# Optimization experiments

Measured on AMD Instinct MI355X. Metric: run time of the kernel, lower is better.

Reference implementation:

```python
import jax, jax.numpy as jnp
import numpy as np

DEPTH = 9            # tree depth -> 2**DEPTH-1 = 511 nodes, 255 internal
ENSEMBLE = 16
CLASS_NUM = 10
IN_DIM = 784
HID = 128            # encode_feature_dimension for arch='mlp'
BATCH = 8192
INTERNAL = 2 ** (DEPTH - 1) - 1   # 255
TOTAL = 2 ** DEPTH - 1            # 511


def setup_inputs() -> dict:
    key = jax.random.key(0)
    ks = jax.random.split(key, 7)
    X = jax.random.normal(ks[0], (BATCH, IN_DIM), dtype=jnp.float32)
    W1 = jax.random.normal(ks[1], (IN_DIM, HID), dtype=jnp.float32) * 0.02
    b1 = jnp.zeros((HID,), jnp.float32)
    W2 = jax.random.normal(ks[2], (HID, CLASS_NUM), dtype=jnp.float32) * 0.02
    b2 = jnp.zeros((CLASS_NUM,), jnp.float32)
    # xavier-uniform style node weights: Linear(HID, 1) per internal node per tree
    limit = float(np.sqrt(6.0 / (HID + 1)))
    nodeW = jax.random.uniform(ks[3], (ENSEMBLE, INTERNAL, HID), jnp.float32, -limit, limit)
    nodeb = jnp.zeros((ENSEMBLE, INTERNAL), jnp.float32)
    return {"X": X, "W1": W1, "b1": b1, "W2": W2, "b2": b2, "nodeW": nodeW, "nodeb": nodeb}


def _tree_paths(feats, nodeW, nodeb):
    # feats: [B, HID]; nodeW: [T, I, HID]; nodeb: [T, I]
    # decisions for ALL internal nodes in one batched GEMM
    dec = jax.nn.sigmoid(jnp.einsum('bd,tid->tib', feats, nodeW) + nodeb[:, :, None])  # [T, I, B]
    T, I, B = dec.shape
    results = jnp.ones((T, TOTAL, B), feats.dtype)
    # level-wise parallel prefix product down the tree (loop over DEPTH-1 levels only)
    for lvl in range(DEPTH - 1):
        start = 2 ** lvl - 1
        cnt = 2 ** lvl
        parent = results[:, start:start + cnt]          # [T, cnt, B]
        d = dec[:, start:start + cnt]                   # [T, cnt, B]
        # children of parent i are 2i+1 (left: *d) and 2i+2 (right: *(1-d)),
        # contiguous + interleaved starting at 2*start+1 = 2**(lvl+1)-1
        children = jnp.stack([parent * d, parent * (1.0 - d)], axis=2).reshape(T, 2 * cnt, B)
        results = results.at[:, 2 * start + 1: 2 * start + 1 + 2 * cnt].set(children)
    return results  # [T, TOTAL, B]


def reference(X, W1, b1, W2, b2, nodeW, nodeb):
    feats = jax.nn.relu(X @ W1 + b1)          # encoder embedding [B, HID]
    prediction = feats @ W2 + b2              # auxiliary predictor [B, CLASS_NUM]
    all_results = _tree_paths(feats, nodeW, nodeb)  # [T, 2**D-1, B]
    return prediction, all_results
```

## Files before the change

kernel.cpp:

```cpp
#include <hip/hip_runtime.h>
#include <hip/hip_bf16.h>

#define BATCH 8192
#define IN_DIM 784
#define HID 128
#define CLS 10
#define ENSEMBLE 16
#define INTERNAL 255
#define TOTAL 511
#define KPAD 800

typedef __attribute__((ext_vector_type(8))) short short8;
typedef __attribute__((ext_vector_type(4))) float floatx4;


__global__ void convert_kernel(const float* __restrict__ X,
                               const float* __restrict__ W1,
                               const float* __restrict__ nodeW,
                               __hip_bfloat16* __restrict__ Xbf,
                               __hip_bfloat16* __restrict__ W1T,
                               __hip_bfloat16* __restrict__ nWbf) {
  const int N1 = BATCH * KPAD;
  const int N2 = HID * KPAD;
  const int N3 = ENSEMBLE * 256 * HID;
  const int total = N1 + N2 + N3;
  for (int i = blockIdx.x * blockDim.x + threadIdx.x; i < total;
       i += gridDim.x * blockDim.x) {
    if (i < N1) {
      int b = i / KPAD, k = i - b * KPAD;
      float v = (k < IN_DIM) ? X[b * IN_DIM + k] : 0.0f;
      Xbf[i] = __float2bfloat16(v);
    } else if (i < N1 + N2) {
      int j = i - N1;
      int c = j / KPAD, k = j - c * KPAD;
      float v = (k < IN_DIM) ? W1[k * HID + c] : 0.0f;
      W1T[j] = __float2bfloat16(v);
    } else {
      int j = i - N1 - N2;
      int t = j / (256 * HID);
      int r = j - t * 256 * HID;
      int ii = r / HID;
      int d = r - ii * HID;
      float v = (ii < INTERNAL) ? nodeW[(t * INTERNAL + ii) * HID + d] : 0.0f;
      nWbf[j] = __float2bfloat16(v);
    }
  }
}

__global__ __launch_bounds__(128) void feats_kernel(
    const __hip_bfloat16* __restrict__ Xbf,
    const __hip_bfloat16* __restrict__ W1T,
    const float* __restrict__ b1,
    float* __restrict__ feats,
    __hip_bfloat16* __restrict__ featsbf) {
  const int wave = threadIdx.x >> 6;
  const int lane = threadIdx.x & 63;
  const int lo = lane & 15;
  const int q = lane >> 4;
  const int m0 = blockIdx.x * 32 + wave * 16;

  floatx4 acc[8];
#pragma unroll
  for (int nt = 0; nt < 8; nt++) acc[nt] = (floatx4){0.f, 0.f, 0.f, 0.f};

  const short* Xp = (const short*)Xbf;
  const short* Wp = (const short*)W1T;
  for (int ks = 0; ks < KPAD / 32; ks++) {
    const int koff = ks * 32 + q * 8;
    short8 a = *(const short8*)(Xp + (size_t)(m0 + lo) * KPAD + koff);
#pragma unroll
    for (int nt = 0; nt < 8; nt++) {
      short8 b = *(const short8*)(Wp + (size_t)(nt * 16 + lo) * KPAD + koff);
      acc[nt] = __builtin_amdgcn_mfma_f32_16x16x32_bf16(a, b, acc[nt], 0, 0, 0);
    }
  }
#pragma unroll
  for (int nt = 0; nt < 8; nt++) {
    const int c = nt * 16 + lo;
    const float bias = b1[c];
#pragma unroll
    for (int r = 0; r < 4; r++) {
      const int brow = m0 + q * 4 + r;
      float v = acc[nt][r] + bias;
      v = fmaxf(v, 0.0f);
      feats[(size_t)brow * HID + c] = v;
      featsbf[(size_t)brow * HID + c] = __float2bfloat16(v);
    }
  }
}

__global__ void pred_kernel(const float* __restrict__ feats,
                            const float* __restrict__ W2,
                            const float* __restrict__ b2,
                            float* __restrict__ out) {
  int gid = blockIdx.x * blockDim.x + threadIdx.x;
  if (gid >= BATCH * CLS) return;
  int b = gid / CLS, c = gid - b * CLS;
  float acc = b2[c];
  const float* fr = feats + (size_t)b * HID;
#pragma unroll 4
  for (int k = 0; k < HID; k++) acc += fr[k] * W2[k * CLS + c];
  out[gid] = acc;
}

__global__ __launch_bounds__(256) void tree_kernel(
    const __hip_bfloat16* __restrict__ featsbf,
    const __hip_bfloat16* __restrict__ nWbf,
    const float* __restrict__ nodeb,
    float* __restrict__ out ) {
  __shared__ float dec_s[INTERNAL * 32];
  __shared__ float P_s[INTERNAL * 32];

  const int t = blockIdx.y;
  const int b0 = blockIdx.x * 32;
  const int tid = threadIdx.x;
  const int wave = tid >> 6;
  const int lane = tid & 63;
  const int lo = lane & 15;
  const int q = lane >> 4;

  const short* Fp = (const short*)featsbf;
  const short* Np = (const short*)nWbf;

  short8 bfr[2][4];
#pragma unroll
  for (int nt = 0; nt < 2; nt++)
#pragma unroll
    for (int ks = 0; ks < 4; ks++)
      bfr[nt][ks] =
          *(const short8*)(Fp + (size_t)(b0 + nt * 16 + lo) * HID + ks * 32 + q * 8);

#pragma unroll
  for (int mt = 0; mt < 4; mt++) {
    const int ibase = wave * 64 + mt * 16;
    floatx4 acc0 = {0.f, 0.f, 0.f, 0.f};
    floatx4 acc1 = {0.f, 0.f, 0.f, 0.f};
#pragma unroll
    for (int ks = 0; ks < 4; ks++) {
      short8 a = *(const short8*)(Np + (size_t)(t * 256 + ibase + lo) * HID +
                                  ks * 32 + q * 8);
      acc0 = __builtin_amdgcn_mfma_f32_16x16x32_bf16(a, bfr[0][ks], acc0, 0, 0, 0);
      acc1 = __builtin_amdgcn_mfma_f32_16x16x32_bf16(a, bfr[1][ks], acc1, 0, 0, 0);
    }
#pragma unroll
    for (int r = 0; r < 4; r++) {
      const int iloc = ibase + q * 4 + r;
      if (iloc < INTERNAL) {
        const float nb = nodeb[t * INTERNAL + iloc];
        const float x0 = acc0[r] + nb;
        const float x1 = acc1[r] + nb;
        dec_s[iloc * 32 + lo] = 1.0f / (1.0f + __expf(-x0));
        dec_s[iloc * 32 + 16 + lo] = 1.0f / (1.0f + __expf(-x1));
      }
    }
  }
  __syncthreads();

  float* outT = out + (size_t)t * TOTAL * BATCH + b0;
  if (tid < 32) {
    P_s[tid] = 1.0f;
    outT[tid] = 1.0f;
  }
  __syncthreads();

  for (int lvl = 0; lvl < 8; lvl++) {
    const int start = (1 << lvl) - 1;
    const int nchild = 2 << lvl;
    const int items = nchild * 32;
    for (int it = tid; it < items; it += 256) {
      const int c = it >> 5;
      const int b = it & 31;
      const int pnode = start + (c >> 1);
      const float d = dec_s[pnode * 32 + b];
      const float pv = P_s[pnode * 32 + b];
      const float val = pv * ((c & 1) ? (1.0f - d) : d);
      const int cnode = 2 * start + 1 + c;
      outT[(size_t)cnode * BATCH + b] = val;
      if (cnode < INTERNAL) P_s[cnode * 32 + b] = val;
    }
    __syncthreads();
  }
}

extern "C" void kernel_launch(void* const* d_in, const int* in_sizes, int n_in,
                              void* d_out, int out_size, void* d_ws, size_t ws_size,
                              hipStream_t stream) {
  const float* X = (const float*)d_in[0];
  const float* W1 = (const float*)d_in[1];
  const float* b1 = (const float*)d_in[2];
  const float* W2 = (const float*)d_in[3];
  const float* b2 = (const float*)d_in[4];
  const float* nodeW = (const float*)d_in[5];
  const float* nodeb = (const float*)d_in[6];

  float* pred_out = (float*)d_out;
  float* results_out = pred_out + BATCH * CLS;

  char* ws = (char*)d_ws;
  float* feats = (float*)(ws + 0);
  __hip_bfloat16* featsbf = (__hip_bfloat16*)(ws + 4194304);
  __hip_bfloat16* Xbf = (__hip_bfloat16*)(ws + 6291456);
  __hip_bfloat16* W1T = (__hip_bfloat16*)(ws + 19398656);
  __hip_bfloat16* nWbf = (__hip_bfloat16*)(ws + 19603456);

  convert_kernel<<<2048, 256, 0, stream>>>(X, W1, nodeW, Xbf, W1T, nWbf);
  feats_kernel<<<BATCH / 32, 128, 0, stream>>>(Xbf, W1T, b1, feats, featsbf);
  pred_kernel<<<(BATCH * CLS + 255) / 256, 256, 0, stream>>>(feats, W2, b2, pred_out);
  tree_kernel<<<dim3(BATCH / 32, ENSEMBLE), 256, 0, stream>>>(featsbf, nWbf, nodeb,
                                                              results_out);
}
```

Baseline: 389.9 us.

## Fuse X bf16 conversion into encoder GEMM and register-resident tree prefix product

Removes the separate fp32-to-bf16 conversion pass over X by converting inside the encoder MFMA loop. The fp32 feats buffer is dropped, and the predictor now reads bf16 features with W2 staged in shared memory. The tree kernel replaces the per-level loop with shared-memory parent buffers and barriers by a per-thread subtree walk in registers, writing with nontemporal stores. The predictor now works from bf16-rounded features, which loosens precision, and the register-resident subtree raises register pressure.

```diff
diff --git a/kernel.cpp b/kernel.cpp
--- a/kernel.cpp
+++ b/kernel.cpp
@@ -14,92 +14,107 @@
 typedef __attribute__((ext_vector_type(4))) float floatx4;
 
 
-__global__ void convert_kernel(const float* __restrict__ X,
-                               const float* __restrict__ W1,
+__device__ inline short f2bf(float f) {
+  __hip_bfloat16 h = __float2bfloat16(f);
+  return *reinterpret_cast<short*>(&h);
+}
+
+__global__ void convert_kernel(const float* __restrict__ W1,
                                const float* __restrict__ nodeW,
-                               __hip_bfloat16* __restrict__ Xbf,
                                __hip_bfloat16* __restrict__ W1T,
                                __hip_bfloat16* __restrict__ nWbf) {
-  const int N1 = BATCH * KPAD;
   const int N2 = HID * KPAD;
   const int N3 = ENSEMBLE * 256 * HID;
-  const int total = N1 + N2 + N3;
+  const int total = N2 + N3;
   for (int i = blockIdx.x * blockDim.x + threadIdx.x; i < total;
        i += gridDim.x * blockDim.x) {
-    if (i < N1) {
-      int b = i / KPAD, k = i - b * KPAD;
-      float v = (k < IN_DIM) ? X[b * IN_DIM + k] : 0.0f;
-      Xbf[i] = __float2bfloat16(v);
-    } else if (i < N1 + N2) {
-      int j = i - N1;
-      int c = j / KPAD, k = j - c * KPAD;
+    if (i < N2) {
+      int c = i / KPAD, k = i - c * KPAD;
       float v = (k < IN_DIM) ? W1[k * HID + c] : 0.0f;
-      W1T[j] = __float2bfloat16(v);
+      W1T[i] = __float2bfloat16(v);
     } else {
-      int j = i - N1 - N2;
-      int t = j / (256 * HID);
-      int r = j - t * 256 * HID;
-      int ii = r / HID;
-      int d = r - ii * HID;
+      int j = i - N2;
+      int t = j >> 15;
+      int r = j & 32767;
+      int ii = r >> 7;
+      int d = r & 127;
       float v = (ii < INTERNAL) ? nodeW[(t * INTERNAL + ii) * HID + d] : 0.0f;
       nWbf[j] = __float2bfloat16(v);
     }
   }
 }
 
-__global__ __launch_bounds__(128) void feats_kernel(
-    const __hip_bfloat16* __restrict__ Xbf,
+__global__ __launch_bounds__(256) void feats_kernel(
+    const float* __restrict__ X,
     const __hip_bfloat16* __restrict__ W1T,
     const float* __restrict__ b1,
-    float* __restrict__ feats,
     __hip_bfloat16* __restrict__ featsbf) {
   const int wave = threadIdx.x >> 6;
   const int lane = threadIdx.x & 63;
   const int lo = lane & 15;
   const int q = lane >> 4;
-  const int m0 = blockIdx.x * 32 + wave * 16;
-
-  floatx4 acc[8];
-#pragma unroll
-  for (int nt = 0; nt < 8; nt++) acc[nt] = (floatx4){0.f, 0.f, 0.f, 0.f};
-
-  const short* Xp = (const short*)Xbf;
+  const int m0 = blockIdx.x * 16;
+  const int cb = wave * 32;
+
+  floatx4 acc0 = {0.f, 0.f, 0.f, 0.f};
+  floatx4 acc1 = {0.f, 0.f, 0.f, 0.f};
   const short* Wp = (const short*)W1T;
+  const float* Xrow = X + (size_t)(m0 + lo) * IN_DIM;
+
   for (int ks = 0; ks < KPAD / 32; ks++) {
-    const int koff = ks * 32 + q * 8;
-    short8 a = *(const short8*)(Xp + (size_t)(m0 + lo) * KPAD + koff);
-#pragma unroll
-    for (int nt = 0; nt < 8; nt++) {
-      short8 b = *(const short8*)(Wp + (size_t)(nt * 16 + lo) * KPAD + koff);
-      acc[nt] = __builtin_amdgcn_mfma_f32_16x16x32_bf16(a, b, acc[nt], 0, 0, 0);
-    }
-  }
-#pragma unroll
-  for (int nt = 0; nt < 8; nt++) {
-    const int c = nt * 16 + lo;
+    const int k0 = ks * 32 + q * 8;
+    short8 a;
+    if (k0 + 8 <= IN_DIM) {
+      float4 x0 = *(const float4*)(Xrow + k0);
+      float4 x1 = *(const float4*)(Xrow + k0 + 4);
+      a[0] = f2bf(x0.x); a[1] = f2bf(x0.y); a[2] = f2bf(x0.z); a[3] = f2bf(x0.w);
+      a[4] = f2bf(x1.x); a[5] = f2bf(x1.y); a[6] = f2bf(x1.z); a[7] = f2bf(x1.w);
+    } else {
+      a = (short8){0, 0, 0, 0, 0, 0, 0, 0};
+    }
+    short8 b0f = *(const short8*)(Wp + (size_t)(cb + lo) * KPAD + k0);
+    short8 b1f = *(const short8*)(Wp + (size_t)(cb + 16 + lo) * KPAD + k0);
+    acc0 = __builtin_amdgcn_mfma_f32_16x16x32_bf16(a, b0f, acc0, 0, 0, 0);
+    acc1 = __builtin_amdgcn_mfma_f32_16x16x32_bf16(a, b1f, acc1, 0, 0, 0);
+  }
+#pragma unroll
+  for (int nt = 0; nt < 2; nt++) {
+    const floatx4 acc = nt ? acc1 : acc0;
+    const int c = cb + nt * 16 + lo;
     const float bias = b1[c];
 #pragma unroll
     for (int r = 0; r < 4; r++) {
-      const int brow = m0 + q * 4 + r;
-      float v = acc[nt][r] + bias;
-      v = fmaxf(v, 0.0f);
-      feats[(size_t)brow * HID + c] = v;
-      featsbf[(size_t)brow * HID + c] = __float2bfloat16(v);
-    }
-  }
-}
-
-__global__ void pred_kernel(const float* __restrict__ feats,
-                            const float* __restrict__ W2,
-                            const float* __restrict__ b2,
-                            float* __restrict__ out) {
-  int gid = blockIdx.x * blockDim.x + threadIdx.x;
+      const int row = m0 + q * 4 + r;
+      float v = fmaxf(acc[r] + bias, 0.0f);
+      featsbf[(size_t)row * HID + c] = __float2bfloat16(v);
+    }
+  }
+}
+
+__global__ __launch_bounds__(256) void pred_kernel(
+    const __hip_bfloat16* __restrict__ featsbf,
+    const float* __restrict__ W2,
+    const float* __restrict__ b2,
+    float* __restrict__ out) {
+  __shared__ float W2s[HID * CLS];
+  __shared__ float b2s[CLS];
+  for (int i = threadIdx.x; i < HID * CLS; i += 256) W2s[i] = W2[i];
+  if (threadIdx.x < CLS) b2s[threadIdx.x] = b2[threadIdx.x];
+  __syncthreads();
+  int gid = blockIdx.x * 256 + threadIdx.x;
   if (gid >= BATCH * CLS) return;
   int b = gid / CLS, c = gid - b * CLS;
-  float acc = b2[c];
-  const float* fr = feats + (size_t)b * HID;
-#pragma unroll 4
-  for (int k = 0; k < HID; k++) acc += fr[k] * W2[k * CLS + c];
+  const short* fr = (const short*)featsbf + (size_t)b * HID;
+  float acc = b2s[c];
+#pragma unroll
+  for (int kk = 0; kk < HID / 8; kk++) {
+    short8 f8 = *(const short8*)(fr + kk * 8);
+#pragma unroll
+    for (int j = 0; j < 8; j++) {
+      unsigned u = ((unsigned)(unsigned short)f8[j]) << 16;
+      acc += __uint_as_float(u) * W2s[(kk * 8 + j) * CLS + c];
+    }
+  }
   out[gid] = acc;
 }
 
@@ -109,7 +124,6 @@
     const float* __restrict__ nodeb,
     float* __restrict__ out ) {
   __shared__ float dec_s[INTERNAL * 32];
-  __shared__ float P_s[INTERNAL * 32];
 
   const int t = blockIdx.y;
   const int b0 = blockIdx.x * 32;
@@ -147,38 +161,52 @@
       const int iloc = ibase + q * 4 + r;
       if (iloc < INTERNAL) {
         const float nb = nodeb[t * INTERNAL + iloc];
-        const float x0 = acc0[r] + nb;
-        const float x1 = acc1[r] + nb;
-        dec_s[iloc * 32 + lo] = 1.0f / (1.0f + __expf(-x0));
-        dec_s[iloc * 32 + 16 + lo] = 1.0f / (1.0f + __expf(-x1));
+        dec_s[iloc * 32 + lo]      = 1.0f / (1.0f + __expf(-(acc0[r] + nb)));
+        dec_s[iloc * 32 + 16 + lo] = 1.0f / (1.0f + __expf(-(acc1[r] + nb)));
       }
     }
   }
   __syncthreads();
 
-  float* outT = out + (size_t)t * TOTAL * BATCH + b0;
-  if (tid < 32) {
-    P_s[tid] = 1.0f;
-    outT[tid] = 1.0f;
-  }
-  __syncthreads();
-
-  for (int lvl = 0; lvl < 8; lvl++) {
-    const int start = (1 << lvl) - 1;
-    const int nchild = 2 << lvl;
-    const int items = nchild * 32;
-    for (int it = tid; it < items; it += 256) {
-      const int c = it >> 5;
-      const int b = it & 31;
-      const int pnode = start + (c >> 1);
-      const float d = dec_s[pnode * 32 + b];
-      const float pv = P_s[pnode * 32 + b];
-      const float val = pv * ((c & 1) ? (1.0f - d) : d);
-      const int cnode = 2 * start + 1 + c;
-      outT[(size_t)cnode * BATCH + b] = val;
-      if (cnode < INTERNAL) P_s[cnode * 32 + b] = val;
-    }
-    __syncthreads();
+  const int s = tid >> 5;
+  const int b = tid & 31;
+  float* outT = out + (size_t)t * TOTAL * BATCH + b0 + b;
+
+  const float d0 = dec_s[0 * 32 + b];
+  const float p1 = (s & 4) ? (1.0f - d0) : d0;
+  const float d1 = dec_s[(1 + (s >> 2)) * 32 + b];
+  const float p2 = p1 * ((s & 2) ? (1.0f - d1) : d1);
+  const float d2 = dec_s[(3 + (s >> 1)) * 32 + b];
+  const float p3 = p2 * ((s & 1) ? (1.0f - d2) : d2);
+
+  if (s == 0) __builtin_nontemporal_store(1.0f, outT);
+  if ((s & 3) == 0)
+    __builtin_nontemporal_store(p1, outT + (size_t)(1 + (s >> 2)) * BATCH);
+  if ((s & 1) == 0)
+    __builtin_nontemporal_store(p2, outT + (size_t)(3 + (s >> 1)) * BATCH);
+  __builtin_nontemporal_store(p3, outT + (size_t)(7 + s) * BATCH);
+
+  float P[32];
+  P[0] = p3;
+#pragma unroll
+  for (int r = 1; r <= 5; r++) {
+    const int W = 1 << r;
+    float nP[32];
+#pragma unroll
+    for (int i = 0; i < 32; i++) {
+      if (i < W) {
+        const int jp = (s << (r - 1)) + (i >> 1);
+        const int ph = ((1 << (2 + r)) - 1) + jp;
+        const float d = dec_s[ph * 32 + b];
+        const float v = P[i >> 1] * ((i & 1) ? (1.0f - d) : d);
+        nP[i] = v;
+        const int ch = ((1 << (3 + r)) - 1) + (s << r) + i;
+        __builtin_nontemporal_store(v, outT + (size_t)ch * BATCH);
+      }
+    }
+#pragma unroll
+    for (int i = 0; i < 32; i++)
+      if (i < W) P[i] = nP[i];
   }
 }
 
@@ -197,15 +225,13 @@
   float* results_out = pred_out + BATCH * CLS;
 
   char* ws = (char*)d_ws;
-  float* feats = (float*)(ws + 0);
-  __hip_bfloat16* featsbf = (__hip_bfloat16*)(ws + 4194304);
-  __hip_bfloat16* Xbf = (__hip_bfloat16*)(ws + 6291456);
-  __hip_bfloat16* W1T = (__hip_bfloat16*)(ws + 19398656);
-  __hip_bfloat16* nWbf = (__hip_bfloat16*)(ws + 19603456);
-
-  convert_kernel<<<2048, 256, 0, stream>>>(X, W1, nodeW, Xbf, W1T, nWbf);
-  feats_kernel<<<BATCH / 32, 128, 0, stream>>>(Xbf, W1T, b1, feats, featsbf);
-  pred_kernel<<<(BATCH * CLS + 255) / 256, 256, 0, stream>>>(feats, W2, b2, pred_out);
+  __hip_bfloat16* W1T = (__hip_bfloat16*)(ws + 0);
+  __hip_bfloat16* nWbf = (__hip_bfloat16*)(ws + 204800);
+  __hip_bfloat16* featsbf = (__hip_bfloat16*)(ws + 1253376);
+
+  convert_kernel<<<612, 256, 0, stream>>>(W1, nodeW, W1T, nWbf);
+  feats_kernel<<<BATCH / 16, 256, 0, stream>>>(X, W1T, b1, featsbf);
+  pred_kernel<<<(BATCH * CLS + 255) / 256, 256, 0, stream>>>(featsbf, W2, b2, pred_out);
   tree_kernel<<<dim3(BATCH / 32, ENSEMBLE), 256, 0, stream>>>(featsbf, nWbf, nodeb,
                                                               results_out);
 }
```

Result: faster. 343.6 us (-11.9%).
